# Kernel tuning notes

Measured on AMD Instinct MI355X. Metric: run time of the kernel, lower is better.

## Reference

```python
import jax, jax.numpy as jnp
import numpy as np

N_NODES = 50000
N_EDGES = 800000
IN_FEAT = 128
H_FEAT = 64
NUM_HEADS = 4
NEG_SLOPE = 0.2  # DGL GATConv default LeakyReLU slope


def _gat_conv(feat, src, dst, W, attn_l, attn_r, bias, num_heads, out_feats):
    # feat: [N, Din]; W: [Din, H*F]; attn_l/attn_r: [H, F]; bias: [H*F]
    N = feat.shape[0]
    h = (feat @ W).reshape(N, num_heads, out_feats)          # [N, H, F]
    el = jnp.sum(h * attn_l, axis=-1)                        # [N, H]
    er = jnp.sum(h * attn_r, axis=-1)                        # [N, H]
    e = jax.nn.leaky_relu(el[src] + er[dst], NEG_SLOPE)      # [E, H]
    # segment softmax over incoming edges of each destination node
    m = jax.ops.segment_max(e, dst, num_segments=N)          # [N, H]
    ex = jnp.exp(e - m[dst])                                 # [E, H]
    s = jax.ops.segment_sum(ex, dst, num_segments=N)         # [N, H]
    alpha = ex / s[dst]                                      # [E, H]
    # attn_drop omitted (eval-mode deterministic reference)
    msg = h[src] * alpha[:, :, None]                         # [E, H, F]
    out = jax.ops.segment_sum(msg, dst, num_segments=N)      # [N, H, F]
    return out + bias.reshape(1, num_heads, out_feats)


def setup_inputs() -> dict:
    key = jax.random.key(0)
    ks = jax.random.split(key, 16)
    feat = jax.random.normal(ks[0], (N_NODES, IN_FEAT), dtype=jnp.float32)
    src = jax.random.randint(ks[1], (N_EDGES,), 0, N_NODES)
    dst = jax.random.randint(ks[2], (N_EDGES,), 0, N_NODES)
    sc = 0.1
    H, F = NUM_HEADS, H_FEAT
    params = {
        'W1': jax.random.normal(ks[3], (IN_FEAT, H * F), dtype=jnp.float32) * sc,
        'al1': jax.random.normal(ks[4], (H, F), dtype=jnp.float32) * sc,
        'ar1': jax.random.normal(ks[5], (H, F), dtype=jnp.float32) * sc,
        'b1': jnp.zeros((H * F,), dtype=jnp.float32),
        'W2': jax.random.normal(ks[6], (H * F, H * F), dtype=jnp.float32) * sc,
        'al2': jax.random.normal(ks[7], (H, F), dtype=jnp.float32) * sc,
        'ar2': jax.random.normal(ks[8], (H, F), dtype=jnp.float32) * sc,
        'b2': jnp.zeros((H * F,), dtype=jnp.float32),
        'W3': jax.random.normal(ks[9], (H * F, F), dtype=jnp.float32) * sc,
        'al3': jax.random.normal(ks[10], (1, F), dtype=jnp.float32) * sc,
        'ar3': jax.random.normal(ks[11], (1, F), dtype=jnp.float32) * sc,
        'b3': jnp.zeros((F,), dtype=jnp.float32),
    }
    return {'feat': feat, 'src': src, 'dst': dst, **params}


def reference(feat, src, dst, W1, al1, ar1, b1, W2, al2, ar2, b2, W3, al3, ar3, b3):
    h = _gat_conv(feat, src, dst, W1, al1, ar1, b1, NUM_HEADS, H_FEAT)
    h = jax.nn.relu(h.reshape(h.shape[0], -1))               # flatten(1) + relu
    h = _gat_conv(h, src, dst, W2, al2, ar2, b2, NUM_HEADS, H_FEAT)
    h = jax.nn.relu(h.reshape(h.shape[0], -1))
    h = _gat_conv(h, src, dst, W3, al3, ar3, b3, 1, H_FEAT)
    return h.mean(axis=1)                                    # [N, h_feat]
```

## Files before the change

kernel.cpp:

```cpp
#include <hip/hip_runtime.h>
#include <math.h>

#define N_NODES 50000
#define N_EDGES 800000

typedef short bf8 __attribute__((ext_vector_type(8)));
typedef float f4x __attribute__((ext_vector_type(4)));
typedef float f2v __attribute__((ext_vector_type(2)));
typedef unsigned short us8 __attribute__((ext_vector_type(8)));

__device__ __forceinline__ unsigned short f2bf(float x) {
  unsigned u = __float_as_uint(x);
  unsigned r = (u + 0x7fff + ((u >> 16) & 1)) >> 16;
  return (unsigned short)r;
}
__device__ __forceinline__ float bf2f(unsigned short b) {
  return __uint_as_float(((unsigned)b) << 16);
}
__device__ __forceinline__ unsigned pack2(float lo, float hi) {
  return (unsigned)f2bf(lo) | ((unsigned)f2bf(hi) << 16);
}
__device__ __forceinline__ f2v bfpair(unsigned d) {
  f2v r;
  r.x = __uint_as_float(d << 16);
  r.y = __uint_as_float(d & 0xffff0000u);
  return r;
}

template <int ABF16>
__global__ __launch_bounds__(256) void gemm_mfma_k(
    const void* __restrict__ Xv, const float* __restrict__ W,
    unsigned short* __restrict__ Yb, float* __restrict__ el,
    float* __restrict__ er, const float* __restrict__ al,
    const float* __restrict__ ar, int N, int K, int M) {
  __shared__ unsigned short As[128][40];
  __shared__ unsigned short Bs[64][40];
  const int tile_n = blockIdx.x * 128;
  const int cb = blockIdx.y * 64;
  const int t = threadIdx.x;
  const int wave = t >> 6, lane = t & 63;
  const int quad = lane >> 4, l16 = lane & 15;

  f4x acc[2][4];
#pragma unroll
  for (int i = 0; i < 2; ++i)
#pragma unroll
    for (int j = 0; j < 4; ++j) acc[i][j] = (f4x){0.f, 0.f, 0.f, 0.f};

  const int ar_ = t >> 1;
  const int ac0 = (t & 1) * 16;
  const int bn = t & 63;
  const int bkq = t >> 6;

  for (int k0 = 0; k0 < K; k0 += 32) {
    if (ABF16) {
      const unsigned short* Xb = (const unsigned short*)Xv;
      int gr = tile_n + ar_;
      us8 u0 = (us8)0, u1 = (us8)0;
      if (gr < N) {
        const unsigned short* s = Xb + (size_t)gr * K + k0 + ac0;
        u0 = *(const us8*)(s + 0);
        u1 = *(const us8*)(s + 8);
      }
      *(us8*)&As[ar_][ac0] = u0;
      *(us8*)&As[ar_][ac0 + 8] = u1;
    } else {
      const float* X = (const float*)Xv;
      int gr = tile_n + ar_;
      uint4 u0, u1;
      if (gr < N) {
        const float* s = X + (size_t)gr * K + k0 + ac0;
        float4 a = *(const float4*)(s + 0);
        float4 b = *(const float4*)(s + 4);
        float4 c = *(const float4*)(s + 8);
        float4 d = *(const float4*)(s + 12);
        u0 = make_uint4(pack2(a.x, a.y), pack2(a.z, a.w),
                        pack2(b.x, b.y), pack2(b.z, b.w));
        u1 = make_uint4(pack2(c.x, c.y), pack2(c.z, c.w),
                        pack2(d.x, d.y), pack2(d.z, d.w));
      } else {
        u0 = make_uint4(0, 0, 0, 0);
        u1 = make_uint4(0, 0, 0, 0);
      }
      *(uint4*)&As[ar_][ac0] = u0;
      *(uint4*)&As[ar_][ac0 + 8] = u1;
    }
    {
      const float* s = W + (size_t)(k0 + bkq * 8) * M + cb + bn;
      float w0 = s[0 * M], w1 = s[1 * M], w2 = s[2 * M], w3 = s[3 * M];
      float w4 = s[4 * M], w5 = s[5 * M], w6 = s[6 * M], w7 = s[7 * M];
      uint4 u = make_uint4(pack2(w0, w1), pack2(w2, w3), pack2(w4, w5),
                           pack2(w6, w7));
      *(uint4*)&Bs[bn][bkq * 8] = u;
    }
    __syncthreads();
    bf8 afrag[2], bfrag[4];
#pragma unroll
    for (int rt = 0; rt < 2; ++rt)
      afrag[rt] = *(const bf8*)&As[wave * 32 + rt * 16 + l16][quad * 8];
#pragma unroll
    for (int ct = 0; ct < 4; ++ct)
      bfrag[ct] = *(const bf8*)&Bs[ct * 16 + l16][quad * 8];
#pragma unroll
    for (int rt = 0; rt < 2; ++rt)
#pragma unroll
      for (int ct = 0; ct < 4; ++ct)
        acc[rt][ct] = __builtin_amdgcn_mfma_f32_16x16x32_bf16(
            afrag[rt], bfrag[ct], acc[rt][ct], 0, 0, 0);
    __syncthreads();
  }
  const int H = M >> 6;
  const int head = cb >> 6;
  float al4[4], ar4[4];
#pragma unroll
  for (int ct = 0; ct < 4; ++ct) {
    al4[ct] = al[cb + ct * 16 + l16];
    ar4[ct] = ar[cb + ct * 16 + l16];
  }
#pragma unroll
  for (int rt = 0; rt < 2; ++rt) {
#pragma unroll
    for (int r = 0; r < 4; ++r) {
      int row = tile_n + wave * 32 + rt * 16 + quad * 4 + r;
      float pl = 0.f, pr = 0.f;
#pragma unroll
      for (int ct = 0; ct < 4; ++ct) {
        float y = acc[rt][ct][r];
        pl += y * al4[ct];
        pr += y * ar4[ct];
        if (row < N) Yb[(size_t)row * M + cb + ct * 16 + l16] = f2bf(y);
      }
#pragma unroll
      for (int off = 1; off < 16; off <<= 1) {
        pl += __shfl_xor(pl, off);
        pr += __shfl_xor(pr, off);
      }
      if (l16 == 0 && row < N) {
        el[row * H + head] = pl;
        er[row * H + head] = pr;
      }
    }
  }
}

__global__ __launch_bounds__(256) void count_deg_k(
    const int4* __restrict__ dst4, int* __restrict__ deg, int E4) {
  int i = blockIdx.x * blockDim.x + threadIdx.x;
  if (i < E4) {
    int4 d = dst4[i];
    atomicAdd(&deg[d.x], 1);
    atomicAdd(&deg[d.y], 1);
    atomicAdd(&deg[d.z], 1);
    atomicAdd(&deg[d.w], 1);
  }
}

__global__ __launch_bounds__(256) void alloc_rows_k(
    const int* __restrict__ deg, int* __restrict__ rowstart,
    int* __restrict__ cursor, int* __restrict__ gcounter, int N) {
  int i = blockIdx.x * blockDim.x + threadIdx.x;
  int lane = threadIdx.x & 63;
  int d = (i < N) ? deg[i] : 0;
  int x = d;
#pragma unroll
  for (int off = 1; off < 64; off <<= 1) {
    int t = __shfl_up(x, off);
    if (lane >= off) x += t;
  }
  int wsum = __shfl(x, 63);
  int base = 0;
  if (lane == 63) base = atomicAdd(gcounter, wsum);
  base = __shfl(base, 63);
  if (i < N) {
    int mystart = base + x - d;
    rowstart[i] = mystart;
    cursor[i] = mystart;
  }
}

__global__ __launch_bounds__(256) void scatter_k(
    const int4* __restrict__ src4, const int4* __restrict__ dst4,
    int* __restrict__ cursor, int* __restrict__ src_sorted, int E4) {
  int i = blockIdx.x * blockDim.x + threadIdx.x;
  if (i < E4) {
    int4 s = src4[i];
    int4 d = dst4[i];
    int p0 = atomicAdd(&cursor[d.x], 1);
    src_sorted[p0] = s.x;
    int p1 = atomicAdd(&cursor[d.y], 1);
    src_sorted[p1] = s.y;
    int p2 = atomicAdd(&cursor[d.z], 1);
    src_sorted[p2] = s.z;
    int p3 = atomicAdd(&cursor[d.w], 1);
    src_sorted[p3] = s.w;
  }
}

template <int RELU>
__global__ __launch_bounds__(256) void node_agg4_k(
    const unsigned short* __restrict__ hb, const float* __restrict__ el,
    const float* __restrict__ er, const int* __restrict__ rowstart,
    const int* __restrict__ rowend, const int* __restrict__ src_sorted,
    float* __restrict__ albuf, const float* __restrict__ bias,
    unsigned short* __restrict__ outb, int N) {
  int node = blockIdx.x * 4 + (threadIdx.x >> 6);
  int lane = threadIdx.x & 63;
  if (node >= N) return;
  int start = rowstart[node], end = rowend[node];
  int head1 = lane & 3;
  int slot = lane >> 2;
  float er_v = er[node * 4 + head1];
  float ssum = 0.f;
  for (int p = start + slot; p < end; p += 16) {
    int s = src_sorted[p];
    float v = el[s * 4 + head1] + er_v;
    v = (v >= 0.f) ? v : 0.2f * v;
    float ex = __expf(v);
    ssum += ex;
    albuf[p * 4 + head1] = ex;
  }
#pragma unroll
  for (int off = 4; off < 64; off <<= 1) ssum += __shfl_xor(ssum, off);
  float inv_s = (end > start) ? 1.f / ssum : 0.f;
  int eslot = lane >> 5;
  int flane = lane & 31;
  int fo8 = flane << 3;
  int headf = fo8 >> 6;
  float inv_f = __shfl(inv_s, headf);
  __builtin_amdgcn_s_waitcnt(0);
  f2v acc2[4];
#pragma unroll
  for (int q = 0; q < 4; ++q) acc2[q] = (f2v){0.f, 0.f};
  if (end > start) {
    int src_first = src_sorted[start];
    for (int p0 = start; p0 < end; p0 += 8) {
      int sj[4];
      float aj[4];
#pragma unroll
      for (int j = 0; j < 4; ++j) {
        int p = p0 + 2 * j + eslot;
        bool v = p < end;
        sj[j] = v ? src_sorted[p] : src_first;
        aj[j] = v ? albuf[p * 4 + headf] : 0.f;
      }
#pragma unroll
      for (int j = 0; j < 4; ++j) {
        uint4 d = *(const uint4*)(hb + (size_t)sj[j] * 256 + fo8);
        f2v a2 = (f2v){aj[j], aj[j]};
        acc2[0] += bfpair(d.x) * a2;
        acc2[1] += bfpair(d.y) * a2;
        acc2[2] += bfpair(d.z) * a2;
        acc2[3] += bfpair(d.w) * a2;
      }
    }
  }
  float acc[8];
#pragma unroll
  for (int q = 0; q < 4; ++q) {
    acc[2 * q] = acc2[q].x;
    acc[2 * q + 1] = acc2[q].y;
  }
#pragma unroll
  for (int q = 0; q < 8; ++q) acc[q] += __shfl_xor(acc[q], 32);
  if (eslot == 0) {
    us8 o;
#pragma unroll
    for (int q = 0; q < 8; ++q) {
      float v = acc[q] * inv_f + bias[fo8 + q];
      if (RELU) v = fmaxf(v, 0.f);
      o[q] = f2bf(v);
    }
    *(us8*)(outb + (size_t)node * 256 + fo8) = o;
  }
}

__global__ __launch_bounds__(256) void node_agg1_k(
    const unsigned short* __restrict__ hb, const float* __restrict__ el,
    const float* __restrict__ er, const int* __restrict__ rowstart,
    const int* __restrict__ rowend, const int* __restrict__ src_sorted,
    float* __restrict__ albuf, const float* __restrict__ bias,
    float* __restrict__ out, int N) {
  int node = blockIdx.x * 4 + (threadIdx.x >> 6);
  int lane = threadIdx.x & 63;
  if (node >= N) return;
  int start = rowstart[node], end = rowend[node];
  float er_v = er[node];
  float ssum = 0.f;
  for (int p = start + lane; p < end; p += 64) {
    float v = el[src_sorted[p]] + er_v;
    v = (v >= 0.f) ? v : 0.2f * v;
    float ex = __expf(v);
    ssum += ex;
    albuf[p] = ex;
  }
#pragma unroll
  for (int off = 1; off < 64; off <<= 1) ssum += __shfl_xor(ssum, off);
  float inv_s = (end > start) ? 1.f / ssum : 0.f;
  int eslot = lane >> 3;
  int flane = lane & 7;
  int fo8 = flane << 3;
  __builtin_amdgcn_s_waitcnt(0);
  f2v acc2[4];
#pragma unroll
  for (int q = 0; q < 4; ++q) acc2[q] = (f2v){0.f, 0.f};
  if (end > start) {
    int src_first = src_sorted[start];
    for (int p0 = start; p0 < end; p0 += 16) {
      int sj[2];
      float aj[2];
#pragma unroll
      for (int j = 0; j < 2; ++j) {
        int p = p0 + 8 * j + eslot;
        bool v = p < end;
        sj[j] = v ? src_sorted[p] : src_first;
        aj[j] = v ? albuf[p] : 0.f;
      }
#pragma unroll
      for (int j = 0; j < 2; ++j) {
        uint4 d = *(const uint4*)(hb + (size_t)sj[j] * 64 + fo8);
        f2v a2 = (f2v){aj[j], aj[j]};
        acc2[0] += bfpair(d.x) * a2;
        acc2[1] += bfpair(d.y) * a2;
        acc2[2] += bfpair(d.z) * a2;
        acc2[3] += bfpair(d.w) * a2;
      }
    }
  }
  float acc[8];
#pragma unroll
  for (int q = 0; q < 4; ++q) {
    acc[2 * q] = acc2[q].x;
    acc[2 * q + 1] = acc2[q].y;
  }
#pragma unroll
  for (int off = 8; off < 64; off <<= 1)
#pragma unroll
    for (int q = 0; q < 8; ++q) acc[q] += __shfl_xor(acc[q], off);
  if (eslot == 0) {
    float* o = out + (size_t)node * 64 + fo8;
#pragma unroll
    for (int q = 0; q < 8; ++q) o[q] = acc[q] * inv_s + bias[fo8 + q];
  }
}

extern "C" void kernel_launch(void* const* d_in, const int* in_sizes, int n_in,
                              void* d_out, int out_size, void* d_ws,
                              size_t ws_size, hipStream_t stream) {
  const float* feat = (const float*)d_in[0];
  const int* src = (const int*)d_in[1];
  const int* dst = (const int*)d_in[2];
  const float* W1 = (const float*)d_in[3];
  const float* al1 = (const float*)d_in[4];
  const float* ar1 = (const float*)d_in[5];
  const float* b1 = (const float*)d_in[6];
  const float* W2 = (const float*)d_in[7];
  const float* al2 = (const float*)d_in[8];
  const float* ar2 = (const float*)d_in[9];
  const float* b2 = (const float*)d_in[10];
  const float* W3 = (const float*)d_in[11];
  const float* al3 = (const float*)d_in[12];
  const float* ar3 = (const float*)d_in[13];
  const float* b3 = (const float*)d_in[14];
  float* out = (float*)d_out;

  unsigned short* hb = (unsigned short*)d_ws;
  unsigned short* fb = hb + (size_t)N_NODES * 256;
  float* el = (float*)(fb + (size_t)N_NODES * 256);
  float* er = el + (size_t)N_NODES * 4;
  int* rowstart = (int*)(er + (size_t)N_NODES * 4);
  int* cursor = rowstart + N_NODES;
  int* deg = cursor + N_NODES;
  int* gcounter = deg + N_NODES;
  int* src_sorted = gcounter + 1;
  float* albuf = (float*)(src_sorted + N_EDGES);

  const int N = N_NODES, E = N_EDGES;
  const int E4 = E / 4;
  const int GX = (N + 127) / 128;

  hipMemsetAsync(deg, 0, (size_t)(N + 1) * sizeof(int), stream);
  hipLaunchKernelGGL(count_deg_k, dim3((E4 + 255) / 256), dim3(256), 0, stream,
                     (const int4*)dst, deg, E4);
  hipLaunchKernelGGL(alloc_rows_k, dim3((N + 255) / 256), dim3(256), 0, stream,
                     deg, rowstart, cursor, gcounter, N);
  hipLaunchKernelGGL(scatter_k, dim3((E4 + 255) / 256), dim3(256), 0, stream,
                     (const int4*)src, (const int4*)dst, cursor, src_sorted,
                     E4);

  hipLaunchKernelGGL((gemm_mfma_k<0>), dim3(GX, 4), dim3(256), 0, stream, feat,
                     W1, hb, el, er, al1, ar1, N, 128, 256);
  hipLaunchKernelGGL((node_agg4_k<1>), dim3((N + 3) / 4), dim3(256), 0, stream,
                     hb, el, er, rowstart, cursor, src_sorted, albuf, b1, fb,
                     N);

  hipLaunchKernelGGL((gemm_mfma_k<1>), dim3(GX, 4), dim3(256), 0, stream, fb,
                     W2, hb, el, er, al2, ar2, N, 256, 256);
  hipLaunchKernelGGL((node_agg4_k<1>), dim3((N + 3) / 4), dim3(256), 0, stream,
                     hb, el, er, rowstart, cursor, src_sorted, albuf, b2, fb,
                     N);

  hipLaunchKernelGGL((gemm_mfma_k<1>), dim3(GX, 1), dim3(256), 0, stream, fb,
                     W3, hb, el, er, al3, ar3, N, 256, 64);
  hipLaunchKernelGGL(node_agg1_k, dim3((N + 3) / 4), dim3(256), 0, stream, hb,
                     el, er, rowstart, cursor, src_sorted, albuf, b3, out, N);
}
```

Baseline: 424.5 us.

## Fuse edge softmax into aggregation loop, drop albuf round-trip

The node aggregation kernels no longer run a separate pass that computes exp attention weights, writes them to a global albuf array and rereads them. Each lane now computes the LeakyReLU/exp weight inline for the edges it aggregates and keeps a running sum, which is reduced across lanes at the end and used as the softmax normalizer. This removes a global write and read per edge, a second read of src_sorted, and a full waitcnt barrier. In exchange there is some redundant el loading and exp across the lanes sharing a head. No max subtraction is applied, the same as before.

```diff
diff --git a/kernel.cpp b/kernel.cpp
--- a/kernel.cpp
+++ b/kernel.cpp
@@ -201,57 +201,44 @@
     const unsigned short* __restrict__ hb, const float* __restrict__ el,
     const float* __restrict__ er, const int* __restrict__ rowstart,
     const int* __restrict__ rowend, const int* __restrict__ src_sorted,
-    float* __restrict__ albuf, const float* __restrict__ bias,
-    unsigned short* __restrict__ outb, int N) {
+    const float* __restrict__ bias, unsigned short* __restrict__ outb,
+    int N) {
   int node = blockIdx.x * 4 + (threadIdx.x >> 6);
   int lane = threadIdx.x & 63;
   if (node >= N) return;
   int start = rowstart[node], end = rowend[node];
-  int head1 = lane & 3;
-  int slot = lane >> 2;
-  float er_v = er[node * 4 + head1];
-  float ssum = 0.f;
-  for (int p = start + slot; p < end; p += 16) {
-    int s = src_sorted[p];
-    float v = el[s * 4 + head1] + er_v;
-    v = (v >= 0.f) ? v : 0.2f * v;
-    float ex = __expf(v);
-    ssum += ex;
-    albuf[p * 4 + head1] = ex;
-  }
-#pragma unroll
-  for (int off = 4; off < 64; off <<= 1) ssum += __shfl_xor(ssum, off);
-  float inv_s = (end > start) ? 1.f / ssum : 0.f;
   int eslot = lane >> 5;
   int flane = lane & 31;
   int fo8 = flane << 3;
   int headf = fo8 >> 6;
-  float inv_f = __shfl(inv_s, headf);
-  __builtin_amdgcn_s_waitcnt(0);
+  float er_v = er[node * 4 + headf];
   f2v acc2[4];
 #pragma unroll
   for (int q = 0; q < 4; ++q) acc2[q] = (f2v){0.f, 0.f};
-  if (end > start) {
-    int src_first = src_sorted[start];
-    for (int p0 = start; p0 < end; p0 += 8) {
-      int sj[4];
-      float aj[4];
-#pragma unroll
-      for (int j = 0; j < 4; ++j) {
-        int p = p0 + 2 * j + eslot;
-        bool v = p < end;
-        sj[j] = v ? src_sorted[p] : src_first;
-        aj[j] = v ? albuf[p * 4 + headf] : 0.f;
-      }
-#pragma unroll
-      for (int j = 0; j < 4; ++j) {
-        uint4 d = *(const uint4*)(hb + (size_t)sj[j] * 256 + fo8);
-        f2v a2 = (f2v){aj[j], aj[j]};
-        acc2[0] += bfpair(d.x) * a2;
-        acc2[1] += bfpair(d.y) * a2;
-        acc2[2] += bfpair(d.z) * a2;
-        acc2[3] += bfpair(d.w) * a2;
-      }
+  float ssum = 0.f;
+  for (int p0 = start; p0 < end; p0 += 8) {
+    int sj[4];
+    float aj[4];
+#pragma unroll
+    for (int j = 0; j < 4; ++j) {
+      int p = p0 + 2 * j + eslot;
+      bool v = p < end;
+      int s = v ? src_sorted[p] : 0;
+      sj[j] = s;
+      float e = el[s * 4 + headf] + er_v;
+      e = (e >= 0.f) ? e : 0.2f * e;
+      float ex = v ? __expf(e) : 0.f;
+      aj[j] = ex;
+      ssum += ex;
+    }
+#pragma unroll
+    for (int j = 0; j < 4; ++j) {
+      uint4 d = *(const uint4*)(hb + (size_t)sj[j] * 256 + fo8);
+      f2v a2 = (f2v){aj[j], aj[j]};
+      acc2[0] += bfpair(d.x) * a2;
+      acc2[1] += bfpair(d.y) * a2;
+      acc2[2] += bfpair(d.z) * a2;
+      acc2[3] += bfpair(d.w) * a2;
     }
   }
   float acc[8];
@@ -262,11 +249,13 @@
   }
 #pragma unroll
   for (int q = 0; q < 8; ++q) acc[q] += __shfl_xor(acc[q], 32);
+  ssum += __shfl_xor(ssum, 32);
+  float inv = (end > start) ? 1.f / ssum : 0.f;
   if (eslot == 0) {
     us8 o;
 #pragma unroll
     for (int q = 0; q < 8; ++q) {
-      float v = acc[q] * inv_f + bias[fo8 + q];
+      float v = acc[q] * inv + bias[fo8 + q];
       if (RELU) v = fmaxf(v, 0.f);
       o[q] = f2bf(v);
     }
@@ -278,52 +267,42 @@
     const unsigned short* __restrict__ hb, const float* __restrict__ el,
     const float* __restrict__ er, const int* __restrict__ rowstart,
     const int* __restrict__ rowend, const int* __restrict__ src_sorted,
-    float* __restrict__ albuf, const float* __restrict__ bias,
-    float* __restrict__ out, int N) {
+    const float* __restrict__ bias, float* __restrict__ out, int N) {
   int node = blockIdx.x * 4 + (threadIdx.x >> 6);
   int lane = threadIdx.x & 63;
   if (node >= N) return;
   int start = rowstart[node], end = rowend[node];
-  float er_v = er[node];
-  float ssum = 0.f;
-  for (int p = start + lane; p < end; p += 64) {
-    float v = el[src_sorted[p]] + er_v;
-    v = (v >= 0.f) ? v : 0.2f * v;
-    float ex = __expf(v);
-    ssum += ex;
-    albuf[p] = ex;
-  }
-#pragma unroll
-  for (int off = 1; off < 64; off <<= 1) ssum += __shfl_xor(ssum, off);
-  float inv_s = (end > start) ? 1.f / ssum : 0.f;
   int eslot = lane >> 3;
   int flane = lane & 7;
   int fo8 = flane << 3;
-  __builtin_amdgcn_s_waitcnt(0);
+  float er_v = er[node];
   f2v acc2[4];
 #pragma unroll
   for (int q = 0; q < 4; ++q) acc2[q] = (f2v){0.f, 0.f};
-  if (end > start) {
-    int src_first = src_sorted[start];
-    for (int p0 = start; p0 < end; p0 += 16) {
-      int sj[2];
-      float aj[2];
-#pragma unroll
-      for (int j = 0; j < 2; ++j) {
-        int p = p0 + 8 * j + eslot;
-        bool v = p < end;
-        sj[j] = v ? src_sorted[p] : src_first;
-        aj[j] = v ? albuf[p] : 0.f;
-      }
-#pragma unroll
-      for (int j = 0; j < 2; ++j) {
-        uint4 d = *(const uint4*)(hb + (size_t)sj[j] * 64 + fo8);
-        f2v a2 = (f2v){aj[j], aj[j]};
-        acc2[0] += bfpair(d.x) * a2;
-        acc2[1] += bfpair(d.y) * a2;
-        acc2[2] += bfpair(d.z) * a2;
-        acc2[3] += bfpair(d.w) * a2;
-      }
+  float ssum = 0.f;
+  for (int p0 = start; p0 < end; p0 += 16) {
+    int sj[2];
+    float aj[2];
+#pragma unroll
+    for (int j = 0; j < 2; ++j) {
+      int p = p0 + 8 * j + eslot;
+      bool v = p < end;
+      int s = v ? src_sorted[p] : 0;
+      sj[j] = s;
+      float e = el[s] + er_v;
+      e = (e >= 0.f) ? e : 0.2f * e;
+      float ex = v ? __expf(e) : 0.f;
+      aj[j] = ex;
+      ssum += ex;
+    }
+#pragma unroll
+    for (int j = 0; j < 2; ++j) {
+      uint4 d = *(const uint4*)(hb + (size_t)sj[j] * 64 + fo8);
+      f2v a2 = (f2v){aj[j], aj[j]};
+      acc2[0] += bfpair(d.x) * a2;
+      acc2[1] += bfpair(d.y) * a2;
+      acc2[2] += bfpair(d.z) * a2;
+      acc2[3] += bfpair(d.w) * a2;
     }
   }
   float acc[8];
@@ -333,13 +312,16 @@
     acc[2 * q + 1] = acc2[q].y;
   }
 #pragma unroll
-  for (int off = 8; off < 64; off <<= 1)
+  for (int off = 8; off < 64; off <<= 1) {
+    ssum += __shfl_xor(ssum, off);
 #pragma unroll
     for (int q = 0; q < 8; ++q) acc[q] += __shfl_xor(acc[q], off);
+  }
+  float inv = (end > start) ? 1.f / ssum : 0.f;
   if (eslot == 0) {
     float* o = out + (size_t)node * 64 + fo8;
 #pragma unroll
-    for (int q = 0; q < 8; ++q) o[q] = acc[q] * inv_s + bias[fo8 + q];
+    for (int q = 0; q < 8; ++q) o[q] = acc[q] * inv + bias[fo8 + q];
   }
 }
 
@@ -372,7 +354,6 @@
   int* deg = cursor + N_NODES;
   int* gcounter = deg + N_NODES;
   int* src_sorted = gcounter + 1;
-  float* albuf = (float*)(src_sorted + N_EDGES);
 
   const int N = N_NODES, E = N_EDGES;
   const int E4 = E / 4;
@@ -390,17 +371,15 @@
   hipLaunchKernelGGL((gemm_mfma_k<0>), dim3(GX, 4), dim3(256), 0, stream, feat,
                      W1, hb, el, er, al1, ar1, N, 128, 256);
   hipLaunchKernelGGL((node_agg4_k<1>), dim3((N + 3) / 4), dim3(256), 0, stream,
-                     hb, el, er, rowstart, cursor, src_sorted, albuf, b1, fb,
-                     N);
+                     hb, el, er, rowstart, cursor, src_sorted, b1, fb, N);
 
   hipLaunchKernelGGL((gemm_mfma_k<1>), dim3(GX, 4), dim3(256), 0, stream, fb,
                      W2, hb, el, er, al2, ar2, N, 256, 256);
   hipLaunchKernelGGL((node_agg4_k<1>), dim3((N + 3) / 4), dim3(256), 0, stream,
-                     hb, el, er, rowstart, cursor, src_sorted, albuf, b2, fb,
-                     N);
+                     hb, el, er, rowstart, cursor, src_sorted, b2, fb, N);
 
   hipLaunchKernelGGL((gemm_mfma_k<1>), dim3(GX, 1), dim3(256), 0, stream, fb,
                      W3, hb, el, er, al3, ar3, N, 256, 64);
   hipLaunchKernelGGL(node_agg1_k, dim3((N + 3) / 4), dim3(256), 0, stream, hb,
-                     el, er, rowstart, cursor, src_sorted, albuf, b3, out, N);
-}
+                     el, er, rowstart, cursor, src_sorted, b3, out, N);
+}
```

New measurement: 428.4 us. Within noise of the previous version (+0.9%).
